# Performance work log

Measured on AMD Instinct MI355X. Metric: run time of the kernel, lower is better.

The kernel has to match this reference:

```python
import jax, jax.numpy as jnp
import numpy as np

GN_EPS = 1e-6
NUM_GROUPS = 32


def group_norm(x, gamma, beta):
    # x: [B,H,W,C], normalize per-sample over (H,W, C//G) within each of G groups
    B, H, W, C = x.shape
    G = NUM_GROUPS
    xg = x.reshape(B, H, W, G, C // G)
    mean = jnp.mean(xg, axis=(1, 2, 4), keepdims=True)
    var = jnp.var(xg, axis=(1, 2, 4), keepdims=True)
    xg = (xg - mean) * jax.lax.rsqrt(var + GN_EPS)
    x = xg.reshape(B, H, W, C)
    return x * gamma + beta


def setup_inputs() -> dict:
    key = jax.random.key(0)
    ks = jax.random.split(key, 6)
    B, H, W, C = 4, 64, 64, 512
    scale = 1.0 / np.sqrt(C)
    return {
        "x": jax.random.normal(ks[0], (B, H, W, C), jnp.float32),
        "gn_gamma": jnp.ones((C,), jnp.float32),
        "gn_beta": jnp.zeros((C,), jnp.float32),
        "Wq": jax.random.normal(ks[1], (C, C), jnp.float32) * scale,
        "bq": jnp.zeros((C,), jnp.float32),
        "Wk": jax.random.normal(ks[2], (C, C), jnp.float32) * scale,
        "bk": jnp.zeros((C,), jnp.float32),
        "Wv": jax.random.normal(ks[3], (C, C), jnp.float32) * scale,
        "bv": jnp.zeros((C,), jnp.float32),
        "Wo": jax.random.normal(ks[4], (C, C), jnp.float32) * scale,
        "bo": jnp.zeros((C,), jnp.float32),
    }


def reference(x, gn_gamma, gn_beta, Wq, bq, Wk, bk, Wv, bv, Wo, bo):
    B, H, W, C = x.shape
    h = group_norm(x, gn_gamma, gn_beta)          # [B,H,W,C]
    t = h.reshape(B, H * W, C)                     # flatten spatial tokens
    q = t @ Wq + bq                                # [B,N,C]
    k = t @ Wk + bk
    v = t @ Wv + bv
    scores = jnp.einsum('bnc,bmc->bnm', q, k) * (C ** -0.5)  # [B,N,N]
    attn = jax.nn.softmax(scores, axis=-1)
    out = jnp.einsum('bnm,bmc->bnc', attn, v)      # [B,N,C]
    out = out @ Wo + bo
    return out.reshape(B, H, W, C) + x
```

## Files before the change

kernel.cpp:

```cpp
#include <hip/hip_runtime.h>
#include <stdint.h>

using u16 = unsigned short;
typedef __attribute__((ext_vector_type(8))) short short8;
typedef __attribute__((ext_vector_type(4))) float floatx4;

__device__ __forceinline__ float b2f(u16 s) {
    union { unsigned u; float f; } x; x.u = ((unsigned)s) << 16; return x.f;
}
__device__ __forceinline__ u16 f2b(float f) {
    unsigned u = __float_as_uint(f);
    unsigned r = (u + 0x7fffu + ((u >> 16) & 1u)) >> 16;
    return (u16)r;
}

__device__ __forceinline__ void gl16(const u16* g, u16* l) {
    __builtin_amdgcn_global_load_lds((const __attribute__((address_space(1))) void*)g,
                                     (__attribute__((address_space(3))) void*)l,
                                     16, 0, 0);
}

__global__ __launch_bounds__(256) void gn_stats_k(const float* __restrict__ x,
                                                  float* __restrict__ part) {
    int bid = blockIdx.x;
    int bg = bid >> 2, pt = bid & 3;
    int b = bg >> 5, g = bg & 31;
    const size_t base = (size_t)b * 4096 * 512 + g * 16;
    int t = threadIdx.x;
    float s = 0.f, ss = 0.f;
    for (int it = 0; it < 16; ++it) {
        int vi = pt * 4096 + it * 256 + t;
        int n = vi >> 2;
        int j = (vi & 3) * 4;
        float4 u = *(const float4*)(x + base + (size_t)n * 512 + j);
        s += u.x + u.y + u.z + u.w;
        ss += u.x * u.x + u.y * u.y + u.z * u.z + u.w * u.w;
    }
    for (int off = 32; off; off >>= 1) {
        s  += __shfl_down(s, off, 64);
        ss += __shfl_down(ss, off, 64);
    }
    __shared__ float rs[4], rss[4];
    int lane = t & 63, w = t >> 6;
    if (lane == 0) { rs[w] = s; rss[w] = ss; }
    __syncthreads();
    if (t == 0) {
        part[bg * 8 + pt * 2]     = rs[0] + rs[1] + rs[2] + rs[3];
        part[bg * 8 + pt * 2 + 1] = rss[0] + rss[1] + rss[2] + rss[3];
    }
}

__global__ __launch_bounds__(256) void gn_apply_k(const float* __restrict__ x,
                                                  const float* __restrict__ gamma,
                                                  const float* __restrict__ beta,
                                                  const float* __restrict__ part,
                                                  u16* __restrict__ h) {
    size_t v = (size_t)blockIdx.x * 256 + threadIdx.x;
    size_t e = v * 4;
    int c = (int)(e & 511);
    int b = (int)(e >> 21);
    int g = c >> 4;
    int bg = b * 32 + g;
    float4 p0 = *(const float4*)(part + bg * 8);
    float4 p1 = *(const float4*)(part + bg * 8 + 4);
    float S1 = p0.x + p0.z + p1.x + p1.z;
    float S2 = p0.y + p0.w + p1.y + p1.w;
    float mean = S1 * (1.f / 65536.f);
    float var  = S2 * (1.f / 65536.f) - mean * mean;
    float rstd = rsqrtf(var + 1e-6f);
    float4 xv = *(const float4*)(x + e);
    float4 gv = *(const float4*)(gamma + c);
    float4 bv = *(const float4*)(beta + c);
    ushort4 o;
    o.x = f2b((xv.x - mean) * rstd * gv.x + bv.x);
    o.y = f2b((xv.y - mean) * rstd * gv.y + bv.y);
    o.z = f2b((xv.z - mean) * rstd * gv.z + bv.z);
    o.w = f2b((xv.w - mean) * rstd * gv.w + bv.w);
    *(ushort4*)(h + e) = o;
}

__global__ __launch_bounds__(256) void transpose_f2b4(const float* __restrict__ Wq,
                                                      const float* __restrict__ Wk,
                                                      const float* __restrict__ Wv,
                                                      const float* __restrict__ Wo,
                                                      u16* __restrict__ wqkv_t,
                                                      u16* __restrict__ wo_t) {
    int z = blockIdx.z;
    const float* src = (z == 0) ? Wq : (z == 1) ? Wk : (z == 2) ? Wv : Wo;
    u16* dst = (z < 3) ? wqkv_t + (size_t)z * 512 * 512 : wo_t;
    __shared__ float tile[32][33];
    int tx = threadIdx.x, ty = threadIdx.y;
    int r0 = blockIdx.x * 32, c0 = blockIdx.y * 32;
#pragma unroll
    for (int i = 0; i < 4; ++i)
        tile[ty + i * 8][tx] = src[(size_t)(r0 + ty + i * 8) * 512 + c0 + tx];
    __syncthreads();
#pragma unroll
    for (int i = 0; i < 4; ++i)
        dst[(size_t)(c0 + ty + i * 8) * 512 + r0 + tx] = f2b(tile[tx][ty + i * 8]);
}

__global__ __launch_bounds__(256) void concat_bias_f(const float* __restrict__ bq,
                                                     const float* __restrict__ bk,
                                                     const float* __restrict__ bv,
                                                     float* __restrict__ dst) {
    int i = blockIdx.x * 256 + threadIdx.x;
    const float* src = (i < 512) ? bq : (i < 1024) ? bk : bv;
    dst[i] = src[i & 511];
}

__global__ __launch_bounds__(256) void gemm_bt(const u16* __restrict__ A, int lda,
                                               const u16* __restrict__ B, int ldb,
                                               u16* __restrict__ C, float* __restrict__ Cf,
                                               int ldc,
                                               const float* __restrict__ bias,
                                               const float* __restrict__ resid,
                                               u16* __restrict__ Vt,
                                               int K, float scale) {
    __shared__ u16 As[128 * 64];
    __shared__ u16 Bs[128 * 64];
    const int t = threadIdx.x;
    const int lane = t & 63, w = t >> 6;
    const int wm = (w >> 1) * 64, wn = (w & 1) * 64;
    const int r = lane & 15, q = lane >> 4;
    const int m0 = blockIdx.x * 128;
    const int n0 = blockIdx.y * 128;

    floatx4 acc[4][4];
#pragma unroll
    for (int mi = 0; mi < 4; ++mi)
#pragma unroll
        for (int ni = 0; ni < 4; ++ni) acc[mi][ni] = (floatx4){0.f, 0.f, 0.f, 0.f};

    int srow[4], soff[4];
#pragma unroll
    for (int j = 0; j < 4; ++j) {
        int e = j * 2048 + t * 8;
        srow[j] = e >> 6;
        soff[j] = ((((e >> 3) & 7) ^ (srow[j] & 7)) * 8);
    }
    const int swzA = (r & 7);

    for (int k0 = 0; k0 < K; k0 += 64) {
        __syncthreads();
#pragma unroll
        for (int j = 0; j < 4; ++j) {
            int e = j * 2048 + t * 8;
            gl16(A + (size_t)(m0 + srow[j]) * lda + k0 + soff[j], As + e);
            gl16(B + (size_t)(n0 + srow[j]) * ldb + k0 + soff[j], Bs + e);
        }
        __syncthreads();
#pragma unroll
        for (int kk = 0; kk < 2; ++kk) {
            short8 af[4], bfr[4];
#pragma unroll
            for (int mi = 0; mi < 4; ++mi)
                af[mi] = *(const short8*)(As + (wm + mi * 16 + r) * 64 +
                                          (((kk * 4 + q) ^ swzA) * 8));
#pragma unroll
            for (int ni = 0; ni < 4; ++ni)
                bfr[ni] = *(const short8*)(Bs + (wn + ni * 16 + r) * 64 +
                                           (((kk * 4 + q) ^ swzA) * 8));
#pragma unroll
            for (int mi = 0; mi < 4; ++mi)
#pragma unroll
                for (int ni = 0; ni < 4; ++ni)
                    acc[mi][ni] = __builtin_amdgcn_mfma_f32_16x16x32_bf16(
                        af[mi], bfr[ni], acc[mi][ni], 0, 0, 0);
        }
    }

    const bool vpath = (Vt != nullptr) && (n0 >= 1024);
#pragma unroll
    for (int ni = 0; ni < 4; ++ni) {
        int col = n0 + wn + ni * 16 + r;
        float bv = bias ? bias[col] : 0.f;
#pragma unroll
        for (int mi = 0; mi < 4; ++mi) {
            int rowb = m0 + wm + mi * 16 + q * 4;
            if (vpath) {
                int c = col - 1024;
                int b = rowb >> 12, n = rowb & 4095;
                ushort4 o;
                o.x = f2b(acc[mi][ni][0] * scale + bv);
                o.y = f2b(acc[mi][ni][1] * scale + bv);
                o.z = f2b(acc[mi][ni][2] * scale + bv);
                o.w = f2b(acc[mi][ni][3] * scale + bv);
                *(ushort4*)(Vt + (((size_t)b * 512 + c) << 12) + n) = o;
            } else {
#pragma unroll
                for (int i = 0; i < 4; ++i) {
                    size_t off = (size_t)(rowb + i) * ldc + col;
                    float v = acc[mi][ni][i] * scale + bv;
                    if (resid) v += resid[off];
                    if (Cf) Cf[off] = v;
                    else    C[off] = f2b(v);
                }
            }
        }
    }
}

#define FLASH_SMEM 147968
__global__ __launch_bounds__(512, 2) void flash_k(const u16* __restrict__ qkv,
                                                  const u16* __restrict__ vt,
                                                  u16* __restrict__ ao) {
    extern __shared__ u16 smem[];
    u16* Ks = smem;
    u16* Vs = smem + 32768;
    u16* Pl = smem + 65536;
    float* lex = (float*)(smem + 73728);
    const int t = threadIdx.x;
    const int lane = t & 63, w = t >> 6;
    const int rw = w & 3, kh = w >> 2;
    const int r = lane & 15, q = lane >> 4;
    const int swz = (q ^ ((r >> 1) & 3)) * 8;
    const int b = blockIdx.y, qt = blockIdx.x;
    const u16* qb = qkv + (size_t)b * 4096 * 1536;
    const u16* kb = qb + 512;
    const u16* vb = vt + (size_t)b * 512 * 4096;
    u16* aob = ao + (size_t)b * 4096 * 512;
    const int wch = w * 64;

    auto stageK = [&](int buf, int kt, int g) {
#pragma unroll
        for (int j = 0; j < 4; ++j) {
            int u = t + j * 512;
            int key = (u & 511) >> 2;
            int sub = u >> 9;
            int c = ((u & 3) ^ ((key >> 1) & 3)) * 8;
            gl16(kb + (size_t)(kt * 128 + key) * 1536 + g * 128 + sub * 32 + c,
                 Ks + buf * 16384 + u * 8);
        }
    };
    auto stageV = [&](int buf, int kt, int k) {
#pragma unroll
        for (int j = 0; j < 4; ++j) {
            int u = t + j * 512;
            int ch = u >> 2;
            int c = ((u & 3) ^ ((ch >> 1) & 3)) * 8;
            gl16(vb + (size_t)ch * 4096 + kt * 128 + k * 32 + c,
                 Vs + buf * 16384 + u * 8);
        }
    };

    stageK(0, 0, 0);
    stageV(0, 0, 0);

    const int qrow = qt * 64 + rw * 16 + r;
    short8 Qreg[16];
#pragma unroll
    for (int kit = 0; kit < 16; ++kit)
        Qreg[kit] = *(const short8*)(qb + (size_t)qrow * 1536 + kit * 32 + q * 8);

    floatx4 acc_o[16];
#pragma unroll
    for (int i = 0; i < 16; ++i) acc_o[i] = (floatx4){0.f, 0.f, 0.f, 0.f};
    float l_half = 0.f;
    const float sc2 = 0.06375872f;

    for (int kt = 0; kt < 32; ++kt) {
        floatx4 acc_s[4];
#pragma unroll
        for (int mi = 0; mi < 4; ++mi) acc_s[mi] = (floatx4){0.f, 0.f, 0.f, 0.f};
#pragma unroll
        for (int g = 0; g < 4; ++g) {
            __syncthreads();
            if (g < 3) stageK((g + 1) & 1, kt, g + 1);
            const u16* kbase = Ks + (g & 1) * 16384;
#pragma unroll
            for (int s = 0; s < 4; ++s) {
                const u16* sbase = kbase + s * 4096;
#pragma unroll
                for (int mi = 0; mi < 4; ++mi) {
                    short8 af = *(const short8*)(sbase + (kh * 64 + mi * 16 + r) * 32 + swz);
                    acc_s[mi] = __builtin_amdgcn_mfma_f32_16x16x32_bf16(
                        af, Qreg[g * 4 + s], acc_s[mi], 0, 0, 0);
                }
            }
        }
        float rs = 0.f;
#pragma unroll
        for (int mi = 0; mi < 4; ++mi)
#pragma unroll
            for (int i = 0; i < 4; ++i) {
                float pv = __builtin_amdgcn_exp2f(acc_s[mi][i] * sc2);
                acc_s[mi][i] = pv;
                rs += pv;
            }
        rs += __shfl_xor(rs, 16, 64);
        rs += __shfl_xor(rs, 32, 64);
        l_half += rs;
#pragma unroll
        for (int mi = 0; mi < 4; ++mi) {
            uint2 vv;
            vv.x = (unsigned)f2b(acc_s[mi][0]) | ((unsigned)f2b(acc_s[mi][1]) << 16);
            vv.y = (unsigned)f2b(acc_s[mi][2]) | ((unsigned)f2b(acc_s[mi][3]) << 16);
            *(uint2*)(Pl + (rw * 16 + r) * 128 +
                      (((kh * 8 + 2 * mi + (q >> 1)) ^ (r & 7)) * 8) + (q & 1) * 4) = vv;
        }
#pragma unroll
        for (int k = 0; k < 4; ++k) {
            __syncthreads();
            if (k < 3)        stageV((k + 1) & 1, kt, k + 1);
            else if (kt < 31) stageV(0, kt + 1, 0);
            if (k == 0 && kt < 31) stageK(0, kt + 1, 0);
            short8 ap[4];
#pragma unroll
            for (int mi = 0; mi < 4; ++mi)
                ap[mi] = *(const short8*)(Pl + (mi * 16 + r) * 128 +
                                          (((k * 4 + q) ^ (r & 7)) * 8));
            const u16* vbase = Vs + (k & 1) * 16384;
#pragma unroll
            for (int ni = 0; ni < 4; ++ni) {
                short8 bf = *(const short8*)(vbase + (wch + ni * 16 + r) * 32 + swz);
#pragma unroll
                for (int mi = 0; mi < 4; ++mi)
                    acc_o[mi * 4 + ni] = __builtin_amdgcn_mfma_f32_16x16x32_bf16(
                        ap[mi], bf, acc_o[mi * 4 + ni], 0, 0, 0);
            }
        }
    }
    if (q == 0) lex[w * 16 + r] = l_half;
    __syncthreads();
#pragma unroll
    for (int mi = 0; mi < 4; ++mi) {
        float4 la = *(const float4*)(lex + mi * 16 + q * 4);
        float4 lb = *(const float4*)(lex + 64 + mi * 16 + q * 4);
        float i0 = 1.f / (la.x + lb.x), i1 = 1.f / (la.y + lb.y);
        float i2 = 1.f / (la.z + lb.z), i3 = 1.f / (la.w + lb.w);
        int rowb = qt * 64 + mi * 16 + q * 4;
#pragma unroll
        for (int ni = 0; ni < 4; ++ni) {
            int col = wch + ni * 16 + r;
            aob[(size_t)(rowb + 0) * 512 + col] = f2b(acc_o[mi * 4 + ni][0] * i0);
            aob[(size_t)(rowb + 1) * 512 + col] = f2b(acc_o[mi * 4 + ni][1] * i1);
            aob[(size_t)(rowb + 2) * 512 + col] = f2b(acc_o[mi * 4 + ni][2] * i2);
            aob[(size_t)(rowb + 3) * 512 + col] = f2b(acc_o[mi * 4 + ni][3] * i3);
        }
    }
}

extern "C" void kernel_launch(void* const* d_in, const int* in_sizes, int n_in,
                              void* d_out, int out_size, void* d_ws, size_t ws_size,
                              hipStream_t stream) {
    const float* x     = (const float*)d_in[0];
    const float* gamma = (const float*)d_in[1];
    const float* beta  = (const float*)d_in[2];
    const float* Wq    = (const float*)d_in[3];
    const float* bq    = (const float*)d_in[4];
    const float* Wk    = (const float*)d_in[5];
    const float* bk    = (const float*)d_in[6];
    const float* Wv    = (const float*)d_in[7];
    const float* bv    = (const float*)d_in[8];
    const float* Wo    = (const float*)d_in[9];
    const float* bo    = (const float*)d_in[10];
    float* out = (float*)d_out;

    char* ws = (char*)d_ws;
    float* stats  = (float*)(ws);
    float* bqkv   = (float*)(ws + 4096);
    u16*   wqkv_t = (u16*)(ws + 16384);
    u16*   wo_t   = wqkv_t + (size_t)1536 * 512;
    u16*   h      = wo_t + (size_t)512 * 512;
    u16*   qkv    = h   + (size_t)16384 * 512;
    u16*   vt     = qkv + (size_t)16384 * 1536;
    u16*   ao     = h;

    dim3 tblk(32, 8, 1);
    transpose_f2b4<<<dim3(16, 16, 4), tblk, 0, stream>>>(Wq, Wk, Wv, Wo, wqkv_t, wo_t);
    concat_bias_f<<<6, 256, 0, stream>>>(bq, bk, bv, bqkv);

    gn_stats_k<<<512, 256, 0, stream>>>(x, stats);
    gn_apply_k<<<8192, 256, 0, stream>>>(x, gamma, beta, stats, h);

    gemm_bt<<<dim3(128, 12, 1), 256, 0, stream>>>(h, 512, wqkv_t, 512,
                                                  qkv, nullptr, 1536, bqkv, nullptr,
                                                  vt, 512, 1.0f);
    hipFuncSetAttribute((const void*)flash_k,
                        hipFuncAttributeMaxDynamicSharedMemorySize, FLASH_SMEM);
    flash_k<<<dim3(64, 4, 1), 512, FLASH_SMEM, stream>>>(qkv, vt, ao);

    gemm_bt<<<dim3(128, 4, 1), 256, 0, stream>>>(ao, 512, wo_t, 512,
                                                 nullptr, out, 512, bo, x,
                                                 nullptr, 512, 1.0f);
}
```

Before: 373.3 us.

## Deepen flash K/V prefetch ring with vmcnt waits and fuse preamble kernels

The flash attention loop now stages K in 64-column slices through a 5-slot ring buffer and waits on explicit s_waitcnt vmcnt counts plus bare s_barrier calls instead of __syncthreads. This keeps several asynchronous global-to-LDS loads in flight across the QK and PV phases, so the kernel stalls less on memory. Separately, the weight transpose, bias concat and GroupNorm stats kernels are merged into one launch to cut launch overhead. The counted waits are fragile: a wrong vmcnt value would race silently, and LDS use grows to 160KB per block.

```diff
diff --git a/kernel.cpp b/kernel.cpp
--- a/kernel.cpp
+++ b/kernel.cpp
@@ -20,33 +20,68 @@
                                      16, 0, 0);
 }
 
-__global__ __launch_bounds__(256) void gn_stats_k(const float* __restrict__ x,
+#define VMW(n) asm volatile("s_waitcnt vmcnt(" #n ")" ::: "memory")
+#define LGW()  asm volatile("s_waitcnt lgkmcnt(0)" ::: "memory")
+#define SBAR() __builtin_amdgcn_s_barrier()
+
+__global__ __launch_bounds__(256) void preamble_k(const float* __restrict__ Wq,
+                                                  const float* __restrict__ Wk,
+                                                  const float* __restrict__ Wv,
+                                                  const float* __restrict__ Wo,
+                                                  const float* __restrict__ bq,
+                                                  const float* __restrict__ bk,
+                                                  const float* __restrict__ bv,
+                                                  const float* __restrict__ x,
+                                                  u16* __restrict__ wqkv_t,
+                                                  u16* __restrict__ wo_t,
+                                                  float* __restrict__ bqkv,
                                                   float* __restrict__ part) {
-    int bid = blockIdx.x;
-    int bg = bid >> 2, pt = bid & 3;
-    int b = bg >> 5, g = bg & 31;
-    const size_t base = (size_t)b * 4096 * 512 + g * 16;
-    int t = threadIdx.x;
-    float s = 0.f, ss = 0.f;
-    for (int it = 0; it < 16; ++it) {
-        int vi = pt * 4096 + it * 256 + t;
-        int n = vi >> 2;
-        int j = (vi & 3) * 4;
-        float4 u = *(const float4*)(x + base + (size_t)n * 512 + j);
-        s += u.x + u.y + u.z + u.w;
-        ss += u.x * u.x + u.y * u.y + u.z * u.z + u.w * u.w;
-    }
-    for (int off = 32; off; off >>= 1) {
-        s  += __shfl_down(s, off, 64);
-        ss += __shfl_down(ss, off, 64);
-    }
+    __shared__ float tile[32][33];
     __shared__ float rs[4], rss[4];
-    int lane = t & 63, w = t >> 6;
-    if (lane == 0) { rs[w] = s; rss[w] = ss; }
-    __syncthreads();
-    if (t == 0) {
-        part[bg * 8 + pt * 2]     = rs[0] + rs[1] + rs[2] + rs[3];
-        part[bg * 8 + pt * 2 + 1] = rss[0] + rss[1] + rss[2] + rss[3];
+    const int bid = blockIdx.x;
+    const int t = threadIdx.x;
+    if (bid < 1024) {
+        int z = bid >> 8, y = (bid >> 4) & 15, xb = bid & 15;
+        const float* src = (z == 0) ? Wq : (z == 1) ? Wk : (z == 2) ? Wv : Wo;
+        u16* dst = (z < 3) ? wqkv_t + (size_t)z * 512 * 512 : wo_t;
+        int tx = t & 31, ty = t >> 5;
+        int r0 = xb * 32, c0 = y * 32;
+#pragma unroll
+        for (int i = 0; i < 4; ++i)
+            tile[ty + i * 8][tx] = src[(size_t)(r0 + ty + i * 8) * 512 + c0 + tx];
+        __syncthreads();
+#pragma unroll
+        for (int i = 0; i < 4; ++i)
+            dst[(size_t)(c0 + ty + i * 8) * 512 + r0 + tx] = f2b(tile[tx][ty + i * 8]);
+    } else if (bid < 1030) {
+        int i = (bid - 1024) * 256 + t;
+        const float* src = (i < 512) ? bq : (i < 1024) ? bk : bv;
+        bqkv[i] = src[i & 511];
+    } else {
+        int bid2 = bid - 1030;
+        int bg = bid2 >> 2, pt = bid2 & 3;
+        int b = bg >> 5, g = bg & 31;
+        const size_t base = (size_t)b * 4096 * 512 + g * 16;
+        float s = 0.f, ss = 0.f;
+        for (int it = 0; it < 16; ++it) {
+            int vi = pt * 4096 + it * 256 + t;
+            int n = vi >> 2;
+            int j = (vi & 3) * 4;
+            float4 u = *(const float4*)(x + base + (size_t)n * 512 + j);
+            s += u.x + u.y + u.z + u.w;
+            ss += u.x * u.x + u.y * u.y + u.z * u.z + u.w * u.w;
+        }
+        for (int off = 32; off; off >>= 1) {
+            s  += __shfl_down(s, off, 64);
+            ss += __shfl_down(ss, off, 64);
+        }
+        int lane = t & 63, w = t >> 6;
+        if (lane == 0) { rs[w] = s; rss[w] = ss; }
+        __syncthreads();
+        if (t == 0) {
+            part[bg * 8 + pt * 2]     = rs[0] + rs[1] + rs[2] + rs[3];
+            part[bg * 8 + pt * 2 + 1] = rss[0] + rss[1] + rss[2] + rss[3];
+        }
     }
 }
 
@@ -79,36 +114,6 @@
     *(ushort4*)(h + e) = o;
 }
 
-__global__ __launch_bounds__(256) void transpose_f2b4(const float* __restrict__ Wq,
-                                                      const float* __restrict__ Wk,
-                                                      const float* __restrict__ Wv,
-                                                      const float* __restrict__ Wo,
-                                                      u16* __restrict__ wqkv_t,
-                                                      u16* __restrict__ wo_t) {
-    int z = blockIdx.z;
-    const float* src = (z == 0) ? Wq : (z == 1) ? Wk : (z == 2) ? Wv : Wo;
-    u16* dst = (z < 3) ? wqkv_t + (size_t)z * 512 * 512 : wo_t;
-    __shared__ float tile[32][33];
-    int tx = threadIdx.x, ty = threadIdx.y;
-    int r0 = blockIdx.x * 32, c0 = blockIdx.y * 32;
-#pragma unroll
-    for (int i = 0; i < 4; ++i)
-        tile[ty + i * 8][tx] = src[(size_t)(r0 + ty + i * 8) * 512 + c0 + tx];
-    __syncthreads();
-#pragma unroll
-    for (int i = 0; i < 4; ++i)
-        dst[(size_t)(c0 + ty + i * 8) * 512 + r0 + tx] = f2b(tile[tx][ty + i * 8]);
-}
-
-__global__ __launch_bounds__(256) void concat_bias_f(const float* __restrict__ bq,
-                                                     const float* __restrict__ bk,
-                                                     const float* __restrict__ bv,
-                                                     float* __restrict__ dst) {
-    int i = blockIdx.x * 256 + threadIdx.x;
-    const float* src = (i < 512) ? bq : (i < 1024) ? bk : bv;
-    dst[i] = src[i & 511];
-}
-
 __global__ __launch_bounds__(256) void gemm_bt(const u16* __restrict__ A, int lda,
                                                const u16* __restrict__ B, int ldb,
                                                u16* __restrict__ C, float* __restrict__ Cf,
@@ -201,15 +206,15 @@
     }
 }
 
-#define FLASH_SMEM 147968
+#define FLASH_SMEM 163840
 __global__ __launch_bounds__(512, 2) void flash_k(const u16* __restrict__ qkv,
                                                   const u16* __restrict__ vt,
                                                   u16* __restrict__ ao) {
     extern __shared__ u16 smem[];
     u16* Ks = smem;
-    u16* Vs = smem + 32768;
-    u16* Pl = smem + 65536;
-    float* lex = (float*)(smem + 73728);
+    u16* Vs = smem + 40960;
+    u16* Pl = smem + 73728;
+    float* lex = (float*)Pl;
     const int t = threadIdx.x;
     const int lane = t & 63, w = t >> 6;
     const int rw = w & 3, kh = w >> 2;
@@ -222,36 +227,36 @@
     u16* aob = ao + (size_t)b * 4096 * 512;
     const int wch = w * 64;
 
-    auto stageK = [&](int buf, int kt, int g) {
-#pragma unroll
-        for (int j = 0; j < 4; ++j) {
+    auto stageK = [&](int buf, int kt_, int p_) {
+#pragma unroll
+        for (int j = 0; j < 2; ++j) {
             int u = t + j * 512;
-            int key = (u & 511) >> 2;
+            int key = (u >> 2) & 127;
             int sub = u >> 9;
             int c = ((u & 3) ^ ((key >> 1) & 3)) * 8;
-            gl16(kb + (size_t)(kt * 128 + key) * 1536 + g * 128 + sub * 32 + c,
-                 Ks + buf * 16384 + u * 8);
+            gl16(kb + (size_t)(kt_ * 128 + key) * 1536 + p_ * 64 + sub * 32 + c,
+                 Ks + buf * 8192 + u * 8);
         }
     };
-    auto stageV = [&](int buf, int kt, int k) {
+    auto stageV = [&](int buf, int kt_, int k_) {
 #pragma unroll
         for (int j = 0; j < 4; ++j) {
             int u = t + j * 512;
             int ch = u >> 2;
             int c = ((u & 3) ^ ((ch >> 1) & 3)) * 8;
-            gl16(vb + (size_t)ch * 4096 + kt * 128 + k * 32 + c,
+            gl16(vb + (size_t)ch * 4096 + kt_ * 128 + k_ * 32 + c,
                  Vs + buf * 16384 + u * 8);
         }
     };
-
-    stageK(0, 0, 0);
-    stageV(0, 0, 0);
 
     const int qrow = qt * 64 + rw * 16 + r;
     short8 Qreg[16];
 #pragma unroll
     for (int kit = 0; kit < 16; ++kit)
         Qreg[kit] = *(const short8*)(qb + (size_t)qrow * 1536 + kit * 32 + q * 8);
+
+    stageK(0, 0, 0); stageK(1, 0, 1); stageK(2, 0, 2); stageK(3, 0, 3);
+    stageV(0, 0, 0);
 
     floatx4 acc_o[16];
 #pragma unroll
@@ -259,38 +264,74 @@
     float l_half = 0.f;
     const float sc2 = 0.06375872f;
 
+#define QK_COMPUTE(P, RB)                                                     \
+    { const u16* kbase = Ks + (RB) * 8192;                                    \
+      _Pragma("unroll") for (int s = 0; s < 2; ++s) {                         \
+        const u16* sbase = kbase + s * 4096;                                  \
+        _Pragma("unroll") for (int mi = 0; mi < 4; ++mi) {                    \
+          short8 af = *(const short8*)(sbase + (kh * 64 + mi * 16 + r) * 32 + swz); \
+          acc_s[mi] = __builtin_amdgcn_mfma_f32_16x16x32_bf16(                \
+              af, Qreg[(P) * 2 + s], acc_s[mi], 0, 0, 0);                     \
+        } } }
+
+#define PV_COMPUTE(K)                                                         \
+    { short8 ap[4];                                                           \
+      _Pragma("unroll") for (int mi = 0; mi < 4; ++mi)                        \
+        ap[mi] = *(const short8*)(Pl + (mi * 16 + r) * 128 +                  \
+                                  ((((K) * 4 + q) ^ (r & 7)) * 8));           \
+      const u16* vbase = Vs + ((K) & 1) * 16384;                              \
+      _Pragma("unroll") for (int ni = 0; ni < 4; ++ni) {                      \
+        short8 bf = *(const short8*)(vbase + (wch + ni * 16 + r) * 32 + swz); \
+        _Pragma("unroll") for (int mi = 0; mi < 4; ++mi)                      \
+          acc_o[mi * 4 + ni] = __builtin_amdgcn_mfma_f32_16x16x32_bf16(       \
+              ap[mi], bf, acc_o[mi * 4 + ni], 0, 0, 0);                       \
+      } }
+
     for (int kt = 0; kt < 32; ++kt) {
+        int rb = (kt * 3) % 5;
         floatx4 acc_s[4];
 #pragma unroll
         for (int mi = 0; mi < 4; ++mi) acc_s[mi] = (floatx4){0.f, 0.f, 0.f, 0.f};
-#pragma unroll
-        for (int g = 0; g < 4; ++g) {
-            __syncthreads();
-            if (g < 3) stageK((g + 1) & 1, kt, g + 1);
-            const u16* kbase = Ks + (g & 1) * 16384;
-#pragma unroll
-            for (int s = 0; s < 4; ++s) {
-                const u16* sbase = kbase + s * 4096;
-#pragma unroll
-                for (int mi = 0; mi < 4; ++mi) {
-                    short8 af = *(const short8*)(sbase + (kh * 64 + mi * 16 + r) * 32 + swz);
-                    acc_s[mi] = __builtin_amdgcn_mfma_f32_16x16x32_bf16(
-                        af, Qreg[g * 4 + s], acc_s[mi], 0, 0, 0);
-                }
-            }
-        }
-        float rs = 0.f;
+        VMW(10); SBAR();
+        { int ib = rb ? rb - 1 : 4; stageK(ib, kt, 4); }
+        stageV(1, kt, 1);
+        QK_COMPUTE(0, rb); rb = (rb == 4) ? 0 : rb + 1;
+        VMW(14); SBAR();
+        { int ib = rb ? rb - 1 : 4; stageK(ib, kt, 5); }
+        QK_COMPUTE(1, rb); rb = (rb == 4) ? 0 : rb + 1;
+        VMW(14); SBAR();
+        { int ib = rb ? rb - 1 : 4; stageK(ib, kt, 6); }
+        QK_COMPUTE(2, rb); rb = (rb == 4) ? 0 : rb + 1;
+        VMW(14); SBAR();
+        { int ib = rb ? rb - 1 : 4; stageK(ib, kt, 7); }
+        QK_COMPUTE(3, rb); rb = (rb == 4) ? 0 : rb + 1;
+        VMW(10); SBAR();
+        if (kt < 31) { int ib = rb ? rb - 1 : 4; stageK(ib, kt + 1, 0); }
+        QK_COMPUTE(4, rb); rb = (rb == 4) ? 0 : rb + 1;
+        if (kt < 31) { VMW(6); } else { VMW(4); }
+        SBAR();
+        if (kt < 31) { int ib = rb ? rb - 1 : 4; stageK(ib, kt + 1, 1); }
+        QK_COMPUTE(5, rb); rb = (rb == 4) ? 0 : rb + 1;
+        if (kt < 31) { VMW(6); } else { VMW(2); }
+        SBAR();
+        if (kt < 31) { int ib = rb ? rb - 1 : 4; stageK(ib, kt + 1, 2); }
+        QK_COMPUTE(6, rb); rb = (rb == 4) ? 0 : rb + 1;
+        if (kt < 31) { VMW(6); } else { VMW(0); }
+        SBAR();
+        if (kt < 31) { int ib = rb ? rb - 1 : 4; stageK(ib, kt + 1, 3); }
+        QK_COMPUTE(7, rb);
+        float rsum = 0.f;
 #pragma unroll
         for (int mi = 0; mi < 4; ++mi)
 #pragma unroll
             for (int i = 0; i < 4; ++i) {
                 float pv = __builtin_amdgcn_exp2f(acc_s[mi][i] * sc2);
                 acc_s[mi][i] = pv;
-                rs += pv;
+                rsum += pv;
             }
-        rs += __shfl_xor(rs, 16, 64);
-        rs += __shfl_xor(rs, 32, 64);
-        l_half += rs;
+        rsum += __shfl_xor(rsum, 16, 64);
+        rsum += __shfl_xor(rsum, 32, 64);
+        l_half += rsum;
 #pragma unroll
         for (int mi = 0; mi < 4; ++mi) {
             uint2 vv;
@@ -299,28 +340,22 @@
             *(uint2*)(Pl + (rw * 16 + r) * 128 +
                       (((kh * 8 + 2 * mi + (q >> 1)) ^ (r & 7)) * 8) + (q & 1) * 4) = vv;
         }
-#pragma unroll
-        for (int k = 0; k < 4; ++k) {
-            __syncthreads();
-            if (k < 3)        stageV((k + 1) & 1, kt, k + 1);
-            else if (kt < 31) stageV(0, kt + 1, 0);
-            if (k == 0 && kt < 31) stageK(0, kt + 1, 0);
-            short8 ap[4];
-#pragma unroll
-            for (int mi = 0; mi < 4; ++mi)
-                ap[mi] = *(const short8*)(Pl + (mi * 16 + r) * 128 +
-                                          (((k * 4 + q) ^ (r & 7)) * 8));
-            const u16* vbase = Vs + (k & 1) * 16384;
-#pragma unroll
-            for (int ni = 0; ni < 4; ++ni) {
-                short8 bf = *(const short8*)(vbase + (wch + ni * 16 + r) * 32 + swz);
-#pragma unroll
-                for (int mi = 0; mi < 4; ++mi)
-                    acc_o[mi * 4 + ni] = __builtin_amdgcn_mfma_f32_16x16x32_bf16(
-                        ap[mi], bf, acc_o[mi * 4 + ni], 0, 0, 0);
-            }
-        }
-    }
+        LGW();
+        if (kt < 31) { VMW(20); } else { VMW(12); }
+        SBAR();
+        PV_COMPUTE(0)
+        if (kt < 31) { VMW(14); } else { VMW(6); }
+        SBAR();
+        stageV(0, kt, 2);
+        PV_COMPUTE(1)
+        VMW(0); SBAR();
+        stageV(1, kt, 3);
+        PV_COMPUTE(2)
+        VMW(0); SBAR();
+        if (kt < 31) stageV(0, kt + 1, 0);
+        PV_COMPUTE(3)
+    }
+    __syncthreads();
     if (q == 0) lex[w * 16 + r] = l_half;
     __syncthreads();
 #pragma unroll
@@ -339,6 +374,8 @@
             aob[(size_t)(rowb + 3) * 512 + col] = f2b(acc_o[mi * 4 + ni][3] * i3);
         }
     }
+#undef QK_COMPUTE
+#undef PV_COMPUTE
 }
 
 extern "C" void kernel_launch(void* const* d_in, const int* in_sizes, int n_in,
@@ -367,11 +404,8 @@
     u16*   vt     = qkv + (size_t)16384 * 1536;
     u16*   ao     = h;
 
-    dim3 tblk(32, 8, 1);
-    transpose_f2b4<<<dim3(16, 16, 4), tblk, 0, stream>>>(Wq, Wk, Wv, Wo, wqkv_t, wo_t);
-    concat_bias_f<<<6, 256, 0, stream>>>(bq, bk, bv, bqkv);
-
-    gn_stats_k<<<512, 256, 0, stream>>>(x, stats);
+    preamble_k<<<1542, 256, 0, stream>>>(Wq, Wk, Wv, Wo, bq, bk, bv, x,
+                                         wqkv_t, wo_t, bqkv, stats);
     gn_apply_k<<<8192, 256, 0, stream>>>(x, gamma, beta, stats, h);
 
     gemm_bt<<<dim3(128, 12, 1), 256, 0, stream>>>(h, 512, wqkv_t, 512,
```

After: 365.3 us. 2.1% less time.
